# Performance work log

Measured on AMD Instinct MI355X. Metric: run time of the kernel, lower is better.

## Reference

```python
import jax, jax.numpy as jnp
import numpy as np
from jax import lax

B, C, H, W = 4, 24, 128, 128
R = 7
NUM_CLASSES = 6
MAX_STEPS = 8


def _conv(x, w, b, pad):
    y = lax.conv_general_dilated(x, w, (1, 1), [(pad, pad), (pad, pad)],
                                 dimension_numbers=("NCHW", "OIHW", "NCHW"))
    return y + b[None, :, None, None]


def setup_inputs() -> dict:
    key = jax.random.key(0)
    ks = jax.random.split(key, 16)
    s = 0.05
    inp = {
        "depth_latent": jax.random.normal(ks[0], (B, C, H, W), jnp.float32),
        "texture_features": jax.random.normal(ks[1], (B, 3, H, W), jnp.float32),
        "class_labels": jax.random.randint(ks[2], (B,), 0, NUM_CLASSES),
        # texture_encoder
        "w_te1": jax.random.normal(ks[3], (64, 3, 3, 3), jnp.float32) * s,
        "b_te1": jnp.zeros((64,), jnp.float32),
        "w_te2": jax.random.normal(ks[4], (128, 64, 3, 3), jnp.float32) * s,
        "b_te2": jnp.zeros((128,), jnp.float32),
        # class embedding [num_classes, 128]
        "emb": jax.random.normal(ks[5], (NUM_CLASSES, 128), jnp.float32) * s,
        # fusion_layer: Conv2d(256,256,3) -> Conv2d(256, C*R*R, 1)
        "w_f1": jax.random.normal(ks[6], (256, 256, 3, 3), jnp.float32) * s,
        "b_f1": jnp.zeros((256,), jnp.float32),
        "w_f2": jax.random.normal(ks[7], (C * R * R, 256, 1, 1), jnp.float32) * s,
        "b_f2": jnp.zeros((C * R * R,), jnp.float32),
        # class_gate: Conv2d(128,64,3) -> Conv2d(64,num_classes,1)
        "w_g1": jax.random.normal(ks[8], (64, 128, 3, 3), jnp.float32) * s,
        "b_g1": jnp.zeros((64,), jnp.float32),
        "w_g2": jax.random.normal(ks[9], (NUM_CLASSES, 64, 1, 1), jnp.float32) * s,
        "b_g2": jnp.zeros((NUM_CLASSES,), jnp.float32),
        "class_intensity": jnp.ones((1, NUM_CLASSES, 1, 1), jnp.float32),
    }
    return inp


def _forward(depth_latent, texture_features, class_labels,
             w_te1, b_te1, w_te2, b_te2, emb,
             w_f1, b_f1, w_f2, b_f2,
             w_g1, b_g1, w_g2, b_g2, class_intensity):
    pad = R // 2
    # texture encoder
    tex = jax.nn.relu(_conv(texture_features, w_te1, b_te1, 1))
    tex = jax.nn.relu(_conv(tex, w_te2, b_te2, 1))  # [B,128,H,W]

    # 1-D integer class label path
    class_cond = jax.nn.one_hot(class_labels, NUM_CLASSES, dtype=jnp.float32)[:, :, None, None]  # [B,K,1,1]
    class_emb = emb[class_labels][:, :, None, None]  # [B,128,1,1]

    gate = jax.nn.sigmoid(_conv(jax.nn.relu(_conv(tex, w_g1, b_g1, 1)), w_g2, b_g2, 0))
    class_gate = gate * class_cond  # [B,K,H,W]

    fused = jnp.concatenate([tex, jnp.broadcast_to(class_emb, (tex.shape[0], 128, H, W))], axis=1)
    weights = _conv(jax.nn.relu(_conv(fused, w_f1, b_f1, 1)), w_f2, b_f2, 0)
    weights = weights.reshape(-1, C, R * R, H, W)

    intensity_map = (class_gate * class_intensity).sum(axis=1, keepdims=True)  # [B,1,H,W]
    weights = weights * intensity_map[:, :, None]  # [B,C,R*R,H,W]
    weights = jax.nn.softmax(weights, axis=2)

    def diffusion_step(lat):
        p = jnp.pad(lat, ((0, 0), (0, 0), (pad, pad), (pad, pad)), mode="edge")
        # unfold order: kernel row-major (i*R + j)
        windows = jnp.stack([p[:, :, i:i + H, j:j + W]
                             for i in range(R) for j in range(R)], axis=2)
        return (windows * weights).sum(axis=2)

    enhanced = lax.fori_loop(0, MAX_STEPS, lambda _, lat: diffusion_step(lat), depth_latent)

    condition_map = intensity_map * class_gate.sum(axis=1, keepdims=True)
    return enhanced, class_gate, condition_map


def reference(depth_latent, texture_features, class_labels,
              w_te1, b_te1, w_te2, b_te2, emb,
              w_f1, b_f1, w_f2, b_f2,
              w_g1, b_g1, w_g2, b_g2, class_intensity):
    return _forward(depth_latent, texture_features, class_labels,
                    w_te1, b_te1, w_te2, b_te2, emb,
                    w_f1, b_f1, w_f2, b_f2,
                    w_g1, b_g1, w_g2, b_g2, class_intensity)
```

## Files before the change

### kernel.cpp

```cpp
#include <hip/hip_runtime.h>
#include <hip/hip_bf16.h>
#include <stdint.h>

#define DINL __device__ __forceinline__

DINL float bf2f(__hip_bfloat16 v) { return __bfloat162float(v); }
DINL __hip_bfloat16 f2bf(float v) { return __float2bfloat16(v); }
DINL float bflo(unsigned int u) { return __uint_as_float(u << 16); }
DINL float bfhi(unsigned int u) { return __uint_as_float(u & 0xffff0000u); }

DINL float loadf(float v) { return v; }
DINL float loadf(__hip_bfloat16 v) { return __bfloat162float(v); }

typedef __attribute__((ext_vector_type(8))) short bf16x8;
typedef __attribute__((ext_vector_type(4))) float f32x4;

DINL void gld_lds16(const void* g, void* l) {
  __builtin_amdgcn_global_load_lds(
      (const __attribute__((address_space(1))) unsigned int*)g,
      (__attribute__((address_space(3))) unsigned int*)l, 16, 0, 0);
}

#define O_WTE1 0
#define O_WG2  1792
#define O_SS   2304
#define O_INT  11520
#define BO_W2B   308224u
#define BO_TE2B 1094656u
#define BO_WG1B 1242112u
#define BO_WF1B 1389568u
#define BO_TEX  4194304u
#define BO_F1   20971520u
#define BO_PING 54525952u
#define BO_PONG 60817408u
#define BO_W    67108864u
#define BO_T1   BO_W

__global__ __launch_bounds__(256) void prep_kernel(
    const float* __restrict__ w_te1, const float* __restrict__ w_te2,
    const float* __restrict__ w_g1,  const float* __restrict__ w_f1,
    const float* __restrict__ w_f2,  const float* __restrict__ w_g2,
    const float* __restrict__ emb,   const int* __restrict__ labels,
    float* __restrict__ wsf)
{
  const int gid = blockIdx.x * 256 + threadIdx.x;
  const int stride = gridDim.x * 256;
  const int A0 = 1728, A1 = A0 + 393216, A2 = A1 + 73728, A3 = A2 + 73728,
            A4 = A3 + 294912, A5 = A4 + 384;
  __hip_bfloat16* w2b  = (__hip_bfloat16*)((char*)wsf + BO_W2B);
  __hip_bfloat16* te2b = (__hip_bfloat16*)((char*)wsf + BO_TE2B);
  __hip_bfloat16* g1b  = (__hip_bfloat16*)((char*)wsf + BO_WG1B);
  __hip_bfloat16* f1b  = (__hip_bfloat16*)((char*)wsf + BO_WF1B);
  for (int i = gid; i < A5; i += stride) {
    if (i < A0) {
      int s = i; int o = s / 27; int r = s - o * 27; int ic = r / 9; int t = r - ic * 9;
      wsf[O_WTE1 + (((o >> 5) * 3 + ic) * 9 + t) * 32 + (o & 31)] = w_te1[s];
    } else if (i < A1) {
      int s = i - A0;
      int j = s & 7; int lane = (s >> 3) & 63; int ks = (s >> 9) & 7;
      int mt = (s >> 12) & 3; int c = s >> 14;
      int tap = mt * 16 + (lane & 15);
      int k = ks * 32 + (lane >> 4) * 8 + j;
      float v = (tap < 49) ? w_f2[(c * 49 + tap) * 256 + k] : 0.f;
      w2b[s] = f2bf(v);
    } else if (i < A2) {
      int s = i - A1;
      int k = s & 31; int n = (s >> 5) & 63; int u = s >> 11;
      int t = u % 9; int v = u / 9; int kc = v & 1; int ocg = v >> 1;
      te2b[s] = f2bf(w_te2[((ocg * 64 + n) * 64 + kc * 32 + k) * 9 + t]);
    } else if (i < A3) {
      int s = i - A2;
      int k = s & 31; int n = (s >> 5) & 63; int u = s >> 11;
      int t = u % 9; int kc = u / 9;
      g1b[s] = f2bf(w_g1[(n * 128 + kc * 32 + k) * 9 + t]);
    } else if (i < A4) {
      int s = i - A3;
      int k = s & 31; int n = (s >> 5) & 63; int u = s >> 11;
      int t = u % 9; int v = u / 9; int kc = v & 3; int ocg = v >> 2;
      f1b[s] = f2bf(w_f1[((ocg * 64 + n) * 256 + kc * 32 + k) * 9 + t]);
    } else {
      int s = i - A4;
      wsf[O_WG2 + s] = w_g2[s];
    }
  }
  if (gid < 16384) {
    const int g = gid >> 4, slot = gid & 15;
    const int b = g >> 8, o = g & 255;
    const int lab = labels[b];
    float St[9];
#pragma unroll
    for (int t = 0; t < 9; ++t) St[t] = 0.f;
#pragma unroll 2
    for (int k = 0; k < 8; ++k) {
      const int i = slot * 8 + k;
      const float e = emb[lab * 128 + i];
      const float* wr = w_f1 + (size_t)(o * 256 + 128 + i) * 9;
#pragma unroll
      for (int t = 0; t < 9; ++t) St[t] += wr[t] * e;
    }
#pragma unroll
    for (int d = 1; d < 16; d <<= 1)
#pragma unroll
      for (int t = 0; t < 9; ++t) St[t] += __shfl_xor(St[t], d, 64);
    if (slot == 0) {
#pragma unroll
      for (int ch = 0; ch < 3; ++ch)
#pragma unroll
        for (int cw = 0; cw < 3; ++cw) {
          float sum = 0.f;
#pragma unroll
          for (int t = 0; t < 9; ++t) {
            int kh = t / 3, kw = t - kh * 3;
            bool ok = !(ch == 0 && kh == 0) && !(ch == 2 && kh == 2) &&
                      !(cw == 0 && kw == 0) && !(cw == 2 && kw == 2);
            if (ok) sum += St[t];
          }
          wsf[O_SS + g * 9 + ch * 3 + cw] = sum;
        }
    }
  }
}

template<typename TIn, int ICH, bool PIXMAJOR>
__global__ __launch_bounds__(256, 2) void conv3x3_kernel(
    const TIn* __restrict__ in, const float* __restrict__ wf,
    const float* __restrict__ bias,
    __hip_bfloat16* __restrict__ out, const int och_total)
{
  constexpr int CH = (ICH < 16) ? ICH : 16;
  constexpr int NCHUNK = ICH / CH;
  __shared__ TIn sIn[CH][18][20];
  const int tid = threadIdx.x;
  const int b = blockIdx.z;
  const int ob = blockIdx.y;
  const int och0 = ob * 32;
  const int tileY = blockIdx.x >> 3, tileX = blockIdx.x & 7;
  const int ty = tid >> 4, tx = tid & 15;
  const int h = tileY * 16 + ty, w = tileX * 16 + tx;
  const int h0 = tileY * 16 - 1, w0 = tileX * 16 - 1;

  float acc[32];
#pragma unroll
  for (int o = 0; o < 32; ++o) acc[o] = bias[och0 + o];

  for (int cc = 0; cc < NCHUNK; ++cc) {
    if (cc) __syncthreads();
    for (int e = tid; e < CH * 324; e += 256) {
      int ic = e / 324, r = e - ic * 324;
      int y = r / 18, x = r - y * 18;
      int gh = h0 + y, gw = w0 + x;
      TIn v = TIn(0.f);
      if ((unsigned)gh < 128u && (unsigned)gw < 128u)
        v = in[((b * ICH + cc * CH + ic) << 14) + (gh << 7) + gw];
      sIn[ic][y][x] = v;
    }
    __syncthreads();
#pragma unroll 1
    for (int ic = 0; ic < CH; ++ic) {
      const float* wrow = wf + (ob * ICH + cc * CH + ic) * 288;
#pragma unroll
      for (int t = 0; t < 9; ++t) {
        const int kh = t / 3, kw = t - kh * 3;
        const float v = loadf(sIn[ic][ty + kh][tx + kw]);
#pragma unroll
        for (int o = 0; o < 32; ++o)
          acc[o] = fmaf(wrow[t * 32 + o], v, acc[o]);
      }
    }
  }

  const int pix = (h << 7) + w;
  if constexpr (!PIXMAJOR) {
#pragma unroll
    for (int o = 0; o < 32; ++o)
      out[((b * och_total + och0 + o) << 14) + pix] = f2bf(fmaxf(acc[o], 0.f));
  } else {
    union { uint4 u4[4]; __hip_bfloat16 hh[32]; } pk;
#pragma unroll
    for (int o = 0; o < 32; ++o) pk.hh[o] = f2bf(fmaxf(acc[o], 0.f));
    uint4* dst = reinterpret_cast<uint4*>(out + ((size_t)(b << 14) + pix) * och_total + och0);
#pragma unroll
    for (int i = 0; i < 4; ++i) dst[i] = pk.u4[i];
  }
}

template<int ICH, bool ADD_SS, bool GATE>
__global__ __launch_bounds__(256, 2) void conv3x3_mfma_kernel(
    const __hip_bfloat16* __restrict__ in, const __hip_bfloat16* __restrict__ wb,
    const float* __restrict__ bias, const float* __restrict__ SS,
    __hip_bfloat16* __restrict__ out, const int och_total,
    const float* __restrict__ wg2, const float* __restrict__ b_g2,
    const int* __restrict__ labels, const float* __restrict__ ci,
    float* __restrict__ out_cg, float* __restrict__ out_cond,
    float* __restrict__ inten)
{
  constexpr int NKC = ICH / 32;
  __shared__ __hip_bfloat16 smem[36000];
#define SHX(pos, k) smem[(pos) * 40 + (k)]
#define SWX(t, n, k) smem[12960 + (((t) * 64 + (n)) * 40) + (k)]
  const int tid = threadIdx.x, b = blockIdx.z, ocg = blockIdx.y;
  const int tileY = blockIdx.x >> 3, tileX = blockIdx.x & 7;
  const int h0 = tileY * 16 - 1, w0 = tileX * 16 - 1;
  const int wave = tid >> 6, lane = tid & 63, m16 = lane & 15, quad = lane >> 4;

  f32x4 acc[4][4];
#pragma unroll
  for (int i = 0; i < 4; ++i)
#pragma unroll
    for (int j = 0; j < 4; ++j) acc[i][j] = f32x4{0.f, 0.f, 0.f, 0.f};

  for (int kc = 0; kc < NKC; ++kc) {
    if (kc) __syncthreads();
    for (int e = tid; e < 1296; e += 256) {
      int pos = e >> 2, q = e & 3;
      int y = pos / 18, x = pos - y * 18;
      int gh = h0 + y, gw = w0 + x;
      uint4 v = uint4{0u, 0u, 0u, 0u};
      if ((unsigned)gh < 128u && (unsigned)gw < 128u)
        v = *(const uint4*)(in + ((size_t)((b << 14) + (gh << 7) + gw)) * ICH + kc * 32 + q * 8);
      *(uint4*)&SHX(pos, q * 8) = v;
    }
    const uint4* wsrc = (const uint4*)(wb + ((size_t)(ocg * NKC + kc)) * 9 * 64 * 32);
    for (int e = tid; e < 2304; e += 256) {
      int q = e & 3, n = (e >> 2) & 63, t = e >> 8;
      *(uint4*)&SWX(t, n, q * 8) = wsrc[e];
    }
    __syncthreads();
#pragma unroll
    for (int t = 0; t < 9; ++t) {
      const int dy = t / 3, dx = t - dy * 3;
      bf16x8 bfr[4];
#pragma unroll
      for (int nt = 0; nt < 4; ++nt)
        bfr[nt] = *(const bf16x8*)&SWX(t, nt * 16 + m16, quad * 8);
#pragma unroll
      for (int mi = 0; mi < 4; ++mi) {
        const int py = wave * 4 + mi;
        const bf16x8 afr = *(const bf16x8*)&SHX((py + dy) * 18 + dx + m16, quad * 8);
#pragma unroll
        for (int nt = 0; nt < 4; ++nt)
          acc[mi][nt] = __builtin_amdgcn_mfma_f32_16x16x32_bf16(afr, bfr[nt], acc[mi][nt], 0, 0, 0);
      }
    }
  }

  float bv[4];
#pragma unroll
  for (int nt = 0; nt < 4; ++nt) bv[nt] = bias[ocg * 64 + nt * 16 + m16];

  if constexpr (GATE) {
    __syncthreads();
    __hip_bfloat16* sG = smem;
#pragma unroll
    for (int mi = 0; mi < 4; ++mi)
#pragma unroll
      for (int nt = 0; nt < 4; ++nt) {
        const int och = nt * 16 + m16;
#pragma unroll
        for (int r = 0; r < 4; ++r) {
          const int p = (wave * 4 + mi) * 16 + quad * 4 + r;
          sG[p * 68 + och] = f2bf(fmaxf(acc[mi][nt][r] + bv[nt], 0.f));
        }
      }
    __syncthreads();
    const int p = tid;
    float a6[6];
#pragma unroll
    for (int k = 0; k < 6; ++k) a6[k] = b_g2[k];
#pragma unroll
    for (int i8 = 0; i8 < 8; ++i8) {
      const bf16x8 v8 = *(const bf16x8*)&sG[p * 68 + i8 * 8];
#pragma unroll
      for (int j = 0; j < 8; ++j) {
        const float v = bf2f(((const __hip_bfloat16*)&v8)[j]);
#pragma unroll
        for (int k = 0; k < 6; ++k)
          a6[k] = fmaf(wg2[k * 64 + i8 * 8 + j], v, a6[k]);
      }
    }
    const int lab = labels[b];
    float gate[6], gl = 0.f;
#pragma unroll
    for (int k = 0; k < 6; ++k) {
      gate[k] = 1.f / (1.f + __expf(-a6[k]));
      gl = (k == lab) ? gate[k] : gl;
    }
    const float civ = ci[lab];
    const float it = gl * civ;
    const int h = tileY * 16 + (p >> 4), w = tileX * 16 + (p & 15);
    const int pix = (h << 7) + w;
#pragma unroll
    for (int k = 0; k < 6; ++k)
      out_cg[((b * 6 + k) << 14) + pix] = (k == lab) ? gate[k] : 0.f;
    inten[(b << 14) + pix] = it;
    out_cond[(b << 14) + pix] = it * gl;
    return;
  }

#pragma unroll
  for (int mi = 0; mi < 4; ++mi) {
    const int py = wave * 4 + mi;
    const int h = tileY * 16 + py;
    const int chc = (h == 0) ? 0 : ((h == 127) ? 2 : 1);
#pragma unroll
    for (int nt = 0; nt < 4; ++nt) {
      float sr0 = 0.f, sr1 = 0.f, sr2 = 0.f;
      if constexpr (ADD_SS) {
        const float* sp = SS + ((size_t)(b << 8) + (ocg * 64 + nt * 16 + m16)) * 9;
        sr0 = sp[chc * 3 + 0]; sr1 = sp[chc * 3 + 1]; sr2 = sp[chc * 3 + 2];
      }
      const int och = ocg * 64 + nt * 16 + m16;
#pragma unroll
      for (int r = 0; r < 4; ++r) {
        const int px = quad * 4 + r;
        const int w = tileX * 16 + px;
        float v = acc[mi][nt][r] + bv[nt];
        if constexpr (ADD_SS)
          v += (w == 0) ? sr0 : ((w == 127) ? sr2 : sr1);
        v = fmaxf(v, 0.f);
        out[((size_t)((b << 14) + (h << 7) + w)) * och_total + och] = f2bf(v);
      }
    }
  }
#undef SHX
#undef SWX
}

__global__ __launch_bounds__(256, 3) void gemm_softmax_kernel(
    const __hip_bfloat16* __restrict__ f1, const __hip_bfloat16* __restrict__ w2b,
    const float* __restrict__ b_f2, const float* __restrict__ inten,
    __hip_bfloat16* __restrict__ wout)
{
  __shared__ __hip_bfloat16 sW[2][8192];
  __shared__ __hip_bfloat16 sT[49][136];
  const int tid = threadIdx.x;
  const int pix0 = blockIdx.x * 128;
  const int c0 = blockIdx.y * 8;
  const int wave = tid >> 6, lane = tid & 63;
  const int n16 = lane & 15, quad = lane >> 4;
  const int p0 = pix0 + wave * 16 + n16;
  const int p1 = p0 + 64;

  bf16x8 bfr0[8], bfr1[8];
#pragma unroll
  for (int ks = 0; ks < 8; ++ks) {
    bfr0[ks] = *(const bf16x8*)(f1 + (size_t)p0 * 256 + ks * 32 + quad * 8);
    bfr1[ks] = *(const bf16x8*)(f1 + (size_t)p1 * 256 + ks * 32 + quad * 8);
  }

  const float s0v = inten[p0], s1v = inten[p1];
  const int ob = pix0 >> 14, op = pix0 & 16383;

#define W2U(u) ((const uint4*)(w2b + ((((size_t)c0 + ((u) >> 1)) * 4 + (((u) & 1) << 1)) << 12)))

  {
    const uint4* s0 = W2U(0);
    uint4* d0 = (uint4*)&sW[0][0];
#pragma unroll
    for (int j = 0; j < 4; ++j)
      gld_lds16(s0 + tid + j * 256, d0 + tid + j * 256);
  }
  __syncthreads();

#pragma unroll 1
  for (int cl = 0; cl < 8; ++cl) {
    const int c = c0 + cl;
    f32x4 ac0[4], ac1[4];
#pragma unroll
    for (int mt = 0; mt < 4; ++mt) { ac0[mt] = f32x4{0.f,0.f,0.f,0.f}; ac1[mt] = f32x4{0.f,0.f,0.f,0.f}; }

#pragma unroll
    for (int h = 0; h < 2; ++h) {
      const int u = cl * 2 + h;
      {
        const uint4* sn = W2U(u < 15 ? u + 1 : 15);
        uint4* dn = (uint4*)&sW[(u + 1) & 1][0];
#pragma unroll
        for (int j = 0; j < 4; ++j)
          gld_lds16(sn + tid + j * 256, dn + tid + j * 256);
      }

      const __hip_bfloat16* bufp = &sW[u & 1][0];
#pragma unroll
      for (int ks = 0; ks < 8; ++ks) {
        const bf16x8 a0 = *(const bf16x8*)(bufp + ((ks) * 64 + lane) * 8);
        const bf16x8 a1 = *(const bf16x8*)(bufp + ((8 + ks) * 64 + lane) * 8);
        ac0[h * 2 + 0] = __builtin_amdgcn_mfma_f32_16x16x32_bf16(a0, bfr0[ks], ac0[h * 2 + 0], 0, 0, 0);
        ac1[h * 2 + 0] = __builtin_amdgcn_mfma_f32_16x16x32_bf16(a0, bfr1[ks], ac1[h * 2 + 0], 0, 0, 0);
        ac0[h * 2 + 1] = __builtin_amdgcn_mfma_f32_16x16x32_bf16(a1, bfr0[ks], ac0[h * 2 + 1], 0, 0, 0);
        ac1[h * 2 + 1] = __builtin_amdgcn_mfma_f32_16x16x32_bf16(a1, bfr1[ks], ac1[h * 2 + 1], 0, 0, 0);
      }
      __syncthreads();
    }

#pragma unroll
    for (int g = 0; g < 2; ++g) {
      f32x4* ac = g ? ac1 : ac0;
      const float s = g ? s1v : s0v;
      float mx = -3.4e38f;
#pragma unroll
      for (int mt = 0; mt < 4; ++mt)
#pragma unroll
        for (int r = 0; r < 4; ++r) {
          const int tap = mt * 16 + quad * 4 + r;
          const bool ok = tap < 49;
          const float lv = ok ? (ac[mt][r] + b_f2[c * 49 + (ok ? tap : 0)]) * s : -3.4e38f;
          ac[mt][r] = lv;
          mx = fmaxf(mx, lv);
        }
      mx = fmaxf(mx, __shfl_xor(mx, 16, 64));
      mx = fmaxf(mx, __shfl_xor(mx, 32, 64));
      float sum = 0.f;
#pragma unroll
      for (int mt = 0; mt < 4; ++mt)
#pragma unroll
        for (int r = 0; r < 4; ++r) {
          const float e = __expf(ac[mt][r] - mx);
          ac[mt][r] = e;
          sum += e;
        }
      sum += __shfl_xor(sum, 16, 64);
      sum += __shfl_xor(sum, 32, 64);
      const float rs = 1.f / sum;

      const int px = wave * 16 + n16 + g * 64;
#pragma unroll
      for (int mt = 0; mt < 4; ++mt)
#pragma unroll
        for (int r = 0; r < 4; ++r) {
          const int tap = mt * 16 + quad * 4 + r;
          if (tap < 49) sT[tap][px] = f2bf(ac[mt][r] * rs);
        }
    }
    __syncthreads();

    __hip_bfloat16* wob = wout + (((size_t)(ob * 24 + c) * 49) << 14) + op;
    for (int e = tid; e < 784; e += 256) {
      const int tap = e >> 4, qq = e & 15;
      *(uint4*)(wob + ((size_t)tap << 14) + qq * 8) = *(const uint4*)&sT[tap][qq * 8];
    }
  }
#undef W2U
}

__global__ __launch_bounds__(256) void diff_kernel(
    const float* __restrict__ lin, const __hip_bfloat16* __restrict__ wts,
    float* __restrict__ lout)
{
  __shared__ float sT[14][136];
  const int bc = blockIdx.y;
  const int h0 = blockIdx.x * 8;
  const int tid = threadIdx.x;
  for (int e = tid; e < 14 * 134; e += 256) {
    int y = e / 134, x = e - y * 134;
    int gh = min(max(h0 - 3 + y, 0), 127), gw = min(max(x - 3, 0), 127);
    sT[y][x] = lin[(bc << 14) + (gh << 7) + gw];
  }
  __syncthreads();
  const int tw = (tid & 31) * 4;
  const int ty = tid >> 5;
  const int h = h0 + ty;
  const __hip_bfloat16* wp = wts + (((size_t)bc * 49) << 14) + (h << 7) + tw;
  float a0 = 0.f, a1 = 0.f, a2 = 0.f, a3 = 0.f;
#pragma unroll
  for (int kh = 0; kh < 7; ++kh) {
    const float* row = &sT[ty + kh][tw];
    float r[12];
    *(f32x4*)&r[0] = *(const f32x4*)(row);
    *(f32x4*)&r[4] = *(const f32x4*)(row + 4);
    *(f32x4*)&r[8] = *(const f32x4*)(row + 8);
#pragma unroll
    for (int kw = 0; kw < 7; ++kw) {
      const int t = kh * 7 + kw;
      const uint2 wq = *(const uint2*)(wp + ((size_t)t << 14));
      a0 = fmaf(bflo(wq.x), r[kw],     a0);
      a1 = fmaf(bfhi(wq.x), r[kw + 1], a1);
      a2 = fmaf(bflo(wq.y), r[kw + 2], a2);
      a3 = fmaf(bfhi(wq.y), r[kw + 3], a3);
    }
  }
  *(f32x4*)(lout + (bc << 14) + (h << 7) + tw) = f32x4{a0, a1, a2, a3};
}

extern "C" void kernel_launch(void* const* d_in, const int* in_sizes, int n_in,
                              void* d_out, int out_size, void* d_ws, size_t ws_size,
                              hipStream_t stream)
{
  const float* depth = (const float*)d_in[0];
  const float* texf  = (const float*)d_in[1];
  const int*   labels= (const int*)d_in[2];
  const float* w_te1 = (const float*)d_in[3];
  const float* b_te1 = (const float*)d_in[4];
  const float* w_te2 = (const float*)d_in[5];
  const float* b_te2 = (const float*)d_in[6];
  const float* emb   = (const float*)d_in[7];
  const float* w_f1  = (const float*)d_in[8];
  const float* b_f1  = (const float*)d_in[9];
  const float* w_f2  = (const float*)d_in[10];
  const float* b_f2  = (const float*)d_in[11];
  const float* w_g1  = (const float*)d_in[12];
  const float* b_g1  = (const float*)d_in[13];
  const float* w_g2  = (const float*)d_in[14];
  const float* b_g2  = (const float*)d_in[15];
  const float* ci    = (const float*)d_in[16];

  char*  ws  = (char*)d_ws;
  float* wsf = (float*)d_ws;
  __hip_bfloat16* w2bf  = (__hip_bfloat16*)(ws + BO_W2B);
  __hip_bfloat16* te2bf = (__hip_bfloat16*)(ws + BO_TE2B);
  __hip_bfloat16* g1bf  = (__hip_bfloat16*)(ws + BO_WG1B);
  __hip_bfloat16* f1bf  = (__hip_bfloat16*)(ws + BO_WF1B);
  __hip_bfloat16* tex   = (__hip_bfloat16*)(ws + BO_TEX);
  __hip_bfloat16* f1    = (__hip_bfloat16*)(ws + BO_F1);
  float* ping           = (float*)(ws + BO_PING);
  float* pong           = (float*)(ws + BO_PONG);
  __hip_bfloat16* wts   = (__hip_bfloat16*)(ws + BO_W);
  __hip_bfloat16* t1    = (__hip_bfloat16*)(ws + BO_T1);

  float* out      = (float*)d_out;
  float* out_enh  = out;
  float* out_cg   = out + 1572864;
  float* out_cond = out + 1966080;

  prep_kernel<<<512, 256, 0, stream>>>(w_te1, w_te2, w_g1, w_f1, w_f2, w_g2, emb, labels, wsf);
  conv3x3_kernel<float, 3, true><<<dim3(64, 2, 4), 256, 0, stream>>>(texf, wsf + O_WTE1, b_te1, t1, 64);
  conv3x3_mfma_kernel<64,  false, false><<<dim3(64, 2, 4), 256, 0, stream>>>(
      t1, te2bf, b_te2, nullptr, tex, 128,
      nullptr, nullptr, nullptr, nullptr, nullptr, nullptr, nullptr);
  conv3x3_mfma_kernel<128, false, true><<<dim3(64, 1, 4), 256, 0, stream>>>(
      tex, g1bf, b_g1, nullptr, nullptr, 64,
      wsf + O_WG2, b_g2, labels, ci, out_cg, out_cond, wsf + O_INT);
  conv3x3_mfma_kernel<128, true, false><<<dim3(64, 4, 4), 256, 0, stream>>>(
      tex, f1bf, b_f1, wsf + O_SS, f1, 256,
      nullptr, nullptr, nullptr, nullptr, nullptr, nullptr, nullptr);
  gemm_softmax_kernel<<<dim3(512, 3), 256, 0, stream>>>(f1, w2bf, b_f2, wsf + O_INT, wts);

  dim3 dgrid(16, 96);
  diff_kernel<<<dgrid, 256, 0, stream>>>(depth, wts, ping);
  diff_kernel<<<dgrid, 256, 0, stream>>>(ping, wts, pong);
  diff_kernel<<<dgrid, 256, 0, stream>>>(pong, wts, ping);
  diff_kernel<<<dgrid, 256, 0, stream>>>(ping, wts, pong);
  diff_kernel<<<dgrid, 256, 0, stream>>>(pong, wts, ping);
  diff_kernel<<<dgrid, 256, 0, stream>>>(ping, wts, pong);
  diff_kernel<<<dgrid, 256, 0, stream>>>(pong, wts, ping);
  diff_kernel<<<dgrid, 256, 0, stream>>>(ping, wts, out_enh);
}
```

Measured before the change: 492.3 us.

## Fuse first diffusion step into GEMM-softmax and read weights directly from global

The first diffusion step is folded into the GEMM+softmax kernel: after the softmax weights for a 128-pixel row are staged in shared memory, the kernel loads the edge-padded depth halo and computes the 49-tap weighted sum directly, so one diff_kernel launch and its reread of the weights are gone. The LDS double-buffered async weight staging is replaced by direct global (cache-served) loads of the A fragments. The softmax also skips the fully masked padding taps beyond 49. The trade-off is that every wave now issues its own global weight loads instead of sharing them through LDS, and the fused kernel gets an extra barrier and a small stencil phase per channel.

```diff
diff --git a/kernel.cpp b/kernel.cpp
--- a/kernel.cpp
+++ b/kernel.cpp
@@ -14,12 +14,6 @@
 
 typedef __attribute__((ext_vector_type(8))) short bf16x8;
 typedef __attribute__((ext_vector_type(4))) float f32x4;
-
-DINL void gld_lds16(const void* g, void* l) {
-  __builtin_amdgcn_global_load_lds(
-      (const __attribute__((address_space(1))) unsigned int*)g,
-      (__attribute__((address_space(3))) unsigned int*)l, 16, 0, 0);
-}
 
 #define O_WTE1 0
 #define O_WG2  1792
@@ -329,10 +323,11 @@
 __global__ __launch_bounds__(256, 3) void gemm_softmax_kernel(
     const __hip_bfloat16* __restrict__ f1, const __hip_bfloat16* __restrict__ w2b,
     const float* __restrict__ b_f2, const float* __restrict__ inten,
-    __hip_bfloat16* __restrict__ wout)
+    __hip_bfloat16* __restrict__ wout,
+    const float* __restrict__ depth, float* __restrict__ lat1)
 {
-  __shared__ __hip_bfloat16 sW[2][8192];
   __shared__ __hip_bfloat16 sT[49][136];
+  __shared__ float sL[7][136];
   const int tid = threadIdx.x;
   const int pix0 = blockIdx.x * 128;
   const int c0 = blockIdx.y * 8;
@@ -349,98 +344,103 @@
   }
 
   const float s0v = inten[p0], s1v = inten[p1];
-  const int ob = pix0 >> 14, op = pix0 & 16383;
-
-#define W2U(u) ((const uint4*)(w2b + ((((size_t)c0 + ((u) >> 1)) * 4 + (((u) & 1) << 1)) << 12)))
-
-  {
-    const uint4* s0 = W2U(0);
-    uint4* d0 = (uint4*)&sW[0][0];
-#pragma unroll
-    for (int j = 0; j < 4; ++j)
-      gld_lds16(s0 + tid + j * 256, d0 + tid + j * 256);
-  }
-  __syncthreads();
+  const int b = pix0 >> 14, row = (pix0 >> 7) & 127, op = pix0 & 16383;
 
 #pragma unroll 1
   for (int cl = 0; cl < 8; ++cl) {
     const int c = c0 + cl;
+    const __hip_bfloat16* w2c = w2b + (((size_t)c) << 14) + lane * 8;
+
     f32x4 ac0[4], ac1[4];
 #pragma unroll
     for (int mt = 0; mt < 4; ++mt) { ac0[mt] = f32x4{0.f,0.f,0.f,0.f}; ac1[mt] = f32x4{0.f,0.f,0.f,0.f}; }
 
 #pragma unroll
     for (int h = 0; h < 2; ++h) {
-      const int u = cl * 2 + h;
-      {
-        const uint4* sn = W2U(u < 15 ? u + 1 : 15);
-        uint4* dn = (uint4*)&sW[(u + 1) & 1][0];
-#pragma unroll
-        for (int j = 0; j < 4; ++j)
-          gld_lds16(sn + tid + j * 256, dn + tid + j * 256);
-      }
-
-      const __hip_bfloat16* bufp = &sW[u & 1][0];
 #pragma unroll
       for (int ks = 0; ks < 8; ++ks) {
-        const bf16x8 a0 = *(const bf16x8*)(bufp + ((ks) * 64 + lane) * 8);
-        const bf16x8 a1 = *(const bf16x8*)(bufp + ((8 + ks) * 64 + lane) * 8);
+        const bf16x8 a0 = *(const bf16x8*)(w2c + h * 8192 + ks * 512);
+        const bf16x8 a1 = *(const bf16x8*)(w2c + h * 8192 + ks * 512 + 4096);
         ac0[h * 2 + 0] = __builtin_amdgcn_mfma_f32_16x16x32_bf16(a0, bfr0[ks], ac0[h * 2 + 0], 0, 0, 0);
         ac1[h * 2 + 0] = __builtin_amdgcn_mfma_f32_16x16x32_bf16(a0, bfr1[ks], ac1[h * 2 + 0], 0, 0, 0);
         ac0[h * 2 + 1] = __builtin_amdgcn_mfma_f32_16x16x32_bf16(a1, bfr0[ks], ac0[h * 2 + 1], 0, 0, 0);
         ac1[h * 2 + 1] = __builtin_amdgcn_mfma_f32_16x16x32_bf16(a1, bfr1[ks], ac1[h * 2 + 1], 0, 0, 0);
       }
-      __syncthreads();
-    }
-
+    }
+
+    const float b48 = b_f2[c * 49 + 48];
 #pragma unroll
     for (int g = 0; g < 2; ++g) {
       f32x4* ac = g ? ac1 : ac0;
       const float s = g ? s1v : s0v;
       float mx = -3.4e38f;
 #pragma unroll
-      for (int mt = 0; mt < 4; ++mt)
+      for (int mt = 0; mt < 3; ++mt)
 #pragma unroll
         for (int r = 0; r < 4; ++r) {
-          const int tap = mt * 16 + quad * 4 + r;
-          const bool ok = tap < 49;
-          const float lv = ok ? (ac[mt][r] + b_f2[c * 49 + (ok ? tap : 0)]) * s : -3.4e38f;
+          const float lv = (ac[mt][r] + b_f2[c * 49 + mt * 16 + quad * 4 + r]) * s;
           ac[mt][r] = lv;
           mx = fmaxf(mx, lv);
         }
+      const float v48 = (ac[3][0] + b48) * s;
+      if (quad == 0) mx = fmaxf(mx, v48);
       mx = fmaxf(mx, __shfl_xor(mx, 16, 64));
       mx = fmaxf(mx, __shfl_xor(mx, 32, 64));
       float sum = 0.f;
 #pragma unroll
-      for (int mt = 0; mt < 4; ++mt)
+      for (int mt = 0; mt < 3; ++mt)
 #pragma unroll
         for (int r = 0; r < 4; ++r) {
           const float e = __expf(ac[mt][r] - mx);
           ac[mt][r] = e;
           sum += e;
         }
+      const float e48 = (quad == 0) ? __expf(v48 - mx) : 0.f;
+      sum += e48;
       sum += __shfl_xor(sum, 16, 64);
       sum += __shfl_xor(sum, 32, 64);
       const float rs = 1.f / sum;
 
       const int px = wave * 16 + n16 + g * 64;
 #pragma unroll
-      for (int mt = 0; mt < 4; ++mt)
-#pragma unroll
-        for (int r = 0; r < 4; ++r) {
-          const int tap = mt * 16 + quad * 4 + r;
-          if (tap < 49) sT[tap][px] = f2bf(ac[mt][r] * rs);
-        }
-    }
-    __syncthreads();
-
-    __hip_bfloat16* wob = wout + (((size_t)(ob * 24 + c) * 49) << 14) + op;
+      for (int mt = 0; mt < 3; ++mt)
+#pragma unroll
+        for (int r = 0; r < 4; ++r)
+          sT[mt * 16 + quad * 4 + r][px] = f2bf(ac[mt][r] * rs);
+      if (quad == 0) sT[48][px] = f2bf(e48 * rs);
+    }
+    __syncthreads();
+
+    __hip_bfloat16* wob = wout + (((size_t)(b * 24 + c) * 49) << 14) + op;
     for (int e = tid; e < 784; e += 256) {
       const int tap = e >> 4, qq = e & 15;
       *(uint4*)(wob + ((size_t)tap << 14) + qq * 8) = *(const uint4*)&sT[tap][qq * 8];
     }
-  }
-#undef W2U
+    const float* dch = depth + (((size_t)(b * 24 + c)) << 14);
+    for (int e = tid; e < 938; e += 256) {
+      const int y = e / 134, x = e - y * 134;
+      const int gh = min(max(row - 3 + y, 0), 127);
+      const int gw = min(max(x - 3, 0), 127);
+      sL[y][x] = dch[(gh << 7) + gw];
+    }
+    __syncthreads();
+
+    {
+      const int w = tid >> 1, par = tid & 1;
+      float a = 0.f;
+#pragma unroll
+      for (int i = 0; i < 25; ++i) {
+        const int t = par + 2 * i;
+        if (t < 49) {
+          const int kh = t / 7, kw = t - kh * 7;
+          a = fmaf(bf2f(sT[t][w]), sL[kh][w + kw], a);
+        }
+      }
+      a += __shfl_xor(a, 1, 64);
+      if (!par) lat1[(((size_t)(b * 24 + c)) << 14) + (row << 7) + w] = a;
+    }
+    __syncthreads();
+  }
 }
 
 __global__ __launch_bounds__(256) void diff_kernel(
@@ -533,10 +533,9 @@
   conv3x3_mfma_kernel<128, true, false><<<dim3(64, 4, 4), 256, 0, stream>>>(
       tex, f1bf, b_f1, wsf + O_SS, f1, 256,
       nullptr, nullptr, nullptr, nullptr, nullptr, nullptr, nullptr);
-  gemm_softmax_kernel<<<dim3(512, 3), 256, 0, stream>>>(f1, w2bf, b_f2, wsf + O_INT, wts);
+  gemm_softmax_kernel<<<dim3(512, 3), 256, 0, stream>>>(f1, w2bf, b_f2, wsf + O_INT, wts, depth, ping);
 
   dim3 dgrid(16, 96);
-  diff_kernel<<<dgrid, 256, 0, stream>>>(depth, wts, ping);
   diff_kernel<<<dgrid, 256, 0, stream>>>(ping, wts, pong);
   diff_kernel<<<dgrid, 256, 0, stream>>>(pong, wts, ping);
   diff_kernel<<<dgrid, 256, 0, stream>>>(ping, wts, pong);
```

Result: slower. 555.0 us (+12.7%).
